# Kernel optimization log

Measured on AMD Instinct MI355X. Metric: run time of the kernel, lower is better.

The kernel has to match this reference:

```python
import jax, jax.numpy as jnp
import numpy as np

NEG = -9e15   # mask value used by reference pyGAT implementation
ALPHA = 0.2   # LeakyReLU negative slope
B, N, F_IN, H, F_HID = 131072, 8, 30, 3, 8


def setup_inputs() -> dict:
    key = jax.random.key(0)
    ks = jax.random.split(key, 14)
    x = jax.random.normal(ks[0], (B, N, F_IN), jnp.float32)
    adj = (jax.random.uniform(ks[1], (B, N, N)) > 0.5).astype(jnp.float32)
    adj = jnp.maximum(adj, jnp.eye(N, dtype=jnp.float32))  # self loops

    def init(k, shp, fan):
        return jax.random.normal(k, shp, jnp.float32) * np.float32(1.0 / np.sqrt(fan))

    return {
        "x": x,
        "adj": adj,
        "W_heads": init(ks[2], (H, F_IN, F_HID), F_IN),       # per-head W
        "a_heads": init(ks[3], (H, 2 * F_HID), 2 * F_HID),    # per-head attention vec
        "W_out": init(ks[4], (H * F_HID, 1), H * F_HID),      # out_att W (nclass=1)
        "a_out": init(ks[5], (2,), 2),                          # out_att attention vec
        "mu_W": init(ks[6], (8, 8), 8), "mu_b": jnp.zeros((8,), jnp.float32),
        "sg_W": init(ks[7], (8, 8), 8), "sg_b": jnp.zeros((8,), jnp.float32),
        "v_W": init(ks[8], (1, 8), 8), "v_b": jnp.zeros((1,), jnp.float32),
    }


def _gat(x, adj, W_heads, a_heads, W_out, a_out):
    # --- multi-head layer (concat=True) ---
    Wh = jnp.einsum('bnf,hfo->bhno', x, W_heads)            # [B,H,N,F_HID]
    a1, a2 = a_heads[:, :F_HID], a_heads[:, F_HID:]
    f1 = jnp.einsum('bhno,ho->bhn', Wh, a1)
    f2 = jnp.einsum('bhno,ho->bhn', Wh, a2)
    e = jax.nn.leaky_relu(f1[:, :, :, None] + f2[:, :, None, :], ALPHA)  # [B,H,N,N]
    e = jnp.where(adj[:, None, :, :] > 0, e, NEG)
    att = jax.nn.softmax(e, axis=-1)
    h = jax.nn.elu(jnp.einsum('bhnm,bhmo->bhno', att, Wh))  # [B,H,N,F_HID]
    h = h.transpose(0, 2, 1, 3).reshape(x.shape[0], N, H * F_HID)  # concat heads

    # --- output attention layer (concat=False, nclass=1) ---
    Wh2 = h @ W_out                                          # [B,N,1]
    g1 = Wh2[..., 0] * a_out[0]
    g2 = Wh2[..., 0] * a_out[1]
    e2 = jax.nn.leaky_relu(g1[:, :, None] + g2[:, None, :], ALPHA)  # [B,N,N]
    e2 = jnp.where(adj > 0, e2, NEG)
    att2 = jax.nn.softmax(e2, axis=-1)
    out = jnp.einsum('bnm,bmo->bno', att2, Wh2)              # [B,N,1]
    return jax.nn.elu(out)[..., 0]                            # squeeze(-1) -> [B,8]


def reference(x, adj, W_heads, a_heads, W_out, a_out,
              mu_W, mu_b, sg_W, sg_b, v_W, v_b):
    g = _gat(x, adj, W_heads, a_heads, W_out, a_out)          # [B,8]
    mu = jax.nn.sigmoid(g @ mu_W.T + mu_b)                    # [B,8]
    sigma = jax.nn.softplus(g @ sg_W.T + sg_b) + 0.001        # [B,8]
    value = g @ v_W.T + v_b                                   # [B,1]
    return (mu, sigma, value)
```

## Files before the change

### kernel.cpp

```cpp
#include <hip/hip_runtime.h>
#include <math.h>

#define TPB 512

constexpr int Bn    = 131072;
constexpr float LOG2E = 1.4426950408889634f;

typedef float v2f __attribute__((ext_vector_type(2)));

__global__ __launch_bounds__(TPB)
void gat_ppo_kernel(const float* __restrict__ xg,
                    const float* __restrict__ adjg,
                    const float* __restrict__ Wg,
                    const float* __restrict__ ahg,
                    const float* __restrict__ wog,
                    const float* __restrict__ aog,
                    const float* __restrict__ muWg,
                    const float* __restrict__ mubg,
                    const float* __restrict__ sgWg,
                    const float* __restrict__ sgbg,
                    const float* __restrict__ vWg,
                    const float* __restrict__ vbg,
                    float* __restrict__ outg)
{
    __shared__ float4 tile[8 * 200];

    const int lb = threadIdx.x;
    const int w  = lb >> 6;
    const int g  = (lb & 63) >> 3;
    const int n  = lb & 7;
    const size_t t = (size_t)blockIdx.x * TPB + lb;

    float4* wt4 = tile + w * 200;

    unsigned amask;
    {
        const float4* a4 = (const float4*)(adjg) + t * 2;
        float4 a0 = a4[0], a1 = a4[1];
        amask =  (unsigned)(a0.x > 0.0f)
              | ((unsigned)(a0.y > 0.0f) << 1)
              | ((unsigned)(a0.z > 0.0f) << 2)
              | ((unsigned)(a0.w > 0.0f) << 3)
              | ((unsigned)(a1.x > 0.0f) << 4)
              | ((unsigned)(a1.y > 0.0f) << 5)
              | ((unsigned)(a1.z > 0.0f) << 6)
              | ((unsigned)(a1.w > 0.0f) << 7);
    }

    float x[30];
    {
        const float2* xr = (const float2*)(xg + t * 30);
        #pragma unroll
        for (int k = 0; k < 15; ++k) {
            float2 v = xr[k];
            x[2 * k] = v.x; x[2 * k + 1] = v.y;
        }
    }

    const v2f* Wp = (const v2f*)Wg;
    float wh2 = 0.0f;

    #pragma unroll
    for (int h = 0; h < 3; ++h) {
        v2f acc[4];
        #pragma unroll
        for (int o2 = 0; o2 < 4; ++o2) acc[o2] = (v2f){0.0f, 0.0f};
        #pragma unroll
        for (int f = 0; f < 30; ++f) {
            v2f xf = (v2f){x[f], x[f]};
            #pragma unroll
            for (int o2 = 0; o2 < 4; ++o2)
                acc[o2] = __builtin_elementwise_fma(xf, Wp[h * 120 + f * 4 + o2], acc[o2]);
        }

        float s1 = 0.0f, s2 = 0.0f;
        #pragma unroll
        for (int o2 = 0; o2 < 4; ++o2) {
            s1 = fmaf(acc[o2].x, ahg[h * 16 + 2 * o2],     s1);
            s1 = fmaf(acc[o2].y, ahg[h * 16 + 2 * o2 + 1], s1);
            s2 = fmaf(acc[o2].x, ahg[h * 16 + 8 + 2 * o2],     s2);
            s2 = fmaf(acc[o2].y, ahg[h * 16 + 8 + 2 * o2 + 1], s2);
        }
        float f1h = s1 * LOG2E;
        float f2h = s2 * LOG2E;

        wt4[g * 25 + n * 3]     = (float4){acc[0].x, acc[0].y, acc[1].x, acc[1].y};
        wt4[g * 25 + n * 3 + 1] = (float4){acc[2].x, acc[2].y, acc[3].x, acc[3].y};

        float p[8];
        float s = 0.0f;
        #pragma unroll
        for (int m = 0; m < 8; ++m) {
            float ev = f1h + __shfl(f2h, m, 8);
            ev = fmaxf(ev, 0.2f * ev);
            float pe = ((amask >> m) & 1u) ? __builtin_amdgcn_exp2f(ev) : 0.0f;
            p[m] = pe; s += pe;
        }

        v2f hacc[4];
        #pragma unroll
        for (int o2 = 0; o2 < 4; ++o2) hacc[o2] = (v2f){0.0f, 0.0f};
        #pragma unroll
        for (int m = 0; m < 8; ++m) {
            float4 lo = wt4[g * 25 + m * 3];
            float4 hi = wt4[g * 25 + m * 3 + 1];
            v2f av = (v2f){p[m], p[m]};
            hacc[0] = __builtin_elementwise_fma(av, (v2f){lo.x, lo.y}, hacc[0]);
            hacc[1] = __builtin_elementwise_fma(av, (v2f){lo.z, lo.w}, hacc[1]);
            hacc[2] = __builtin_elementwise_fma(av, (v2f){hi.x, hi.y}, hacc[2]);
            hacc[3] = __builtin_elementwise_fma(av, (v2f){hi.z, hi.w}, hacc[3]);
        }
        float rs = 1.0f / s;
        #pragma unroll
        for (int o2 = 0; o2 < 4; ++o2) {
            #pragma unroll
            for (int j = 0; j < 2; ++j) {
                float hv = hacc[o2][j] * rs;
                hv = (hv > 0.0f) ? hv : (__expf(hv) - 1.0f);
                wh2 = fmaf(hv, wog[h * 8 + 2 * o2 + j], wh2);
            }
        }
    }

    const float a0c = aog[0] * LOG2E, a1c = aog[1] * LOG2E;
    float wh2a[8];
    #pragma unroll
    for (int m = 0; m < 8; ++m) wh2a[m] = __shfl(wh2, m, 8);

    float g1 = a0c * wh2;
    float s2s = 0.0f;
    float og = 0.0f;
    #pragma unroll
    for (int m = 0; m < 8; ++m) {
        float ev = fmaf(a1c, wh2a[m], g1);
        ev = fmaxf(ev, 0.2f * ev);
        float pe = ((amask >> m) & 1u) ? __builtin_amdgcn_exp2f(ev) : 0.0f;
        s2s += pe;
        og = fmaf(pe, wh2a[m], og);
    }
    og /= s2s;
    float g2v = (og > 0.0f) ? og : (__expf(og) - 1.0f);

    v2f gp[4];
    #pragma unroll
    for (int m = 0; m < 4; ++m)
        gp[m] = (v2f){__shfl(g2v, 2 * m, 8), __shfl(g2v, 2 * m + 1, 8)};

    const v2f* muWp = (const v2f*)muWg;
    const v2f* sgWp = (const v2f*)sgWg;
    const v2f* vWp  = (const v2f*)vWg;
    v2f ma = (v2f){0.0f, 0.0f}, sa = (v2f){0.0f, 0.0f}, va = (v2f){0.0f, 0.0f};
    #pragma unroll
    for (int k = 0; k < 4; ++k) {
        ma = __builtin_elementwise_fma(gp[k], muWp[n * 4 + k], ma);
        sa = __builtin_elementwise_fma(gp[k], sgWp[n * 4 + k], sa);
        va = __builtin_elementwise_fma(gp[k], vWp[k],          va);
    }
    float mu = ma.x + ma.y + mubg[n];
    float sg = sa.x + sa.y + sgbg[n];
    float vv = va.x + va.y + vbg[0];

    mu = 1.0f / (1.0f + __expf(-mu));
    sg = fmaxf(sg, 0.0f) + log1pf(__expf(-fabsf(sg))) + 0.001f;

    outg[t]          = mu;
    outg[Bn * 8 + t] = sg;
    if (n == 0) outg[Bn * 16 + (t >> 3)] = vv;
}

extern "C" void kernel_launch(void* const* d_in, const int* in_sizes, int n_in,
                              void* d_out, int out_size, void* d_ws, size_t ws_size,
                              hipStream_t stream) {
    const float* xg   = (const float*)d_in[0];
    const float* adjg = (const float*)d_in[1];
    const float* Wg   = (const float*)d_in[2];
    const float* ahg  = (const float*)d_in[3];
    const float* wog  = (const float*)d_in[4];
    const float* aog  = (const float*)d_in[5];
    const float* muW  = (const float*)d_in[6];
    const float* mub  = (const float*)d_in[7];
    const float* sgW  = (const float*)d_in[8];
    const float* sgb  = (const float*)d_in[9];
    const float* vW   = (const float*)d_in[10];
    const float* vb   = (const float*)d_in[11];
    float* outg = (float*)d_out;

    dim3 grid(Bn * 8 / TPB);
    gat_ppo_kernel<<<grid, TPB, 0, stream>>>(xg, adjg, Wg, ahg, wog, aog,
                                             muW, mub, sgW, sgb, vW, vb, outg);
}
```

Measured before the change: 51.85 us.

## Interleave all three heads per x element and halve block size

The per-head loop is restructured so each x element is loaded once and applied to all three heads' accumulators, with separate shared-memory tiles per head. The float x[30] register array disappears, and the softmax and aggregation phases run for all heads together, which exposes more independent work. Block size drops from 512 to 256 threads. The cost is more live accumulators (24 v2f in flight) and 3x the shared memory per wave, which may limit occupancy.

```diff
diff --git a/kernel.cpp b/kernel.cpp
--- a/kernel.cpp
+++ b/kernel.cpp
@@ -1,7 +1,7 @@
 #include <hip/hip_runtime.h>
 #include <math.h>
 
-#define TPB 512
+#define TPB 256
 
 constexpr int Bn    = 131072;
 constexpr float LOG2E = 1.4426950408889634f;
@@ -23,15 +23,13 @@
                     const float* __restrict__ vbg,
                     float* __restrict__ outg)
 {
-    __shared__ float4 tile[8 * 200];
+    __shared__ float4 tile[4][3][200];
 
     const int lb = threadIdx.x;
     const int w  = lb >> 6;
     const int g  = (lb & 63) >> 3;
     const int n  = lb & 7;
     const size_t t = (size_t)blockIdx.x * TPB + lb;
-
-    float4* wt4 = tile + w * 200;
 
     unsigned amask;
     {
@@ -47,75 +45,98 @@
               | ((unsigned)(a1.w > 0.0f) << 7);
     }
 
-    float x[30];
+    const v2f* Wp = (const v2f*)Wg;
+    v2f acc[3][4];
+    #pragma unroll
+    for (int h = 0; h < 3; ++h)
+        #pragma unroll
+        for (int o2 = 0; o2 < 4; ++o2) acc[h][o2] = (v2f){0.0f, 0.0f};
+
     {
         const float2* xr = (const float2*)(xg + t * 30);
         #pragma unroll
         for (int k = 0; k < 15; ++k) {
             float2 v = xr[k];
-            x[2 * k] = v.x; x[2 * k + 1] = v.y;
-        }
-    }
-
-    const v2f* Wp = (const v2f*)Wg;
+            #pragma unroll
+            for (int e = 0; e < 2; ++e) {
+                const int f = 2 * k + e;
+                const float xf = e ? v.y : v.x;
+                v2f xv = (v2f){xf, xf};
+                #pragma unroll
+                for (int h = 0; h < 3; ++h)
+                    #pragma unroll
+                    for (int o2 = 0; o2 < 4; ++o2)
+                        acc[h][o2] = __builtin_elementwise_fma(xv, Wp[h * 120 + f * 4 + o2], acc[h][o2]);
+            }
+        }
+    }
+
+    float f1h[3], f2h[3];
+    #pragma unroll
+    for (int h = 0; h < 3; ++h) {
+        float s1 = 0.0f, s2 = 0.0f;
+        #pragma unroll
+        for (int o2 = 0; o2 < 4; ++o2) {
+            s1 = fmaf(acc[h][o2].x, ahg[h * 16 + 2 * o2],     s1);
+            s1 = fmaf(acc[h][o2].y, ahg[h * 16 + 2 * o2 + 1], s1);
+            s2 = fmaf(acc[h][o2].x, ahg[h * 16 + 8 + 2 * o2],     s2);
+            s2 = fmaf(acc[h][o2].y, ahg[h * 16 + 8 + 2 * o2 + 1], s2);
+        }
+        f1h[h] = s1 * LOG2E;
+        f2h[h] = s2 * LOG2E;
+    }
+
+    #pragma unroll
+    for (int h = 0; h < 3; ++h) {
+        tile[w][h][g * 25 + n * 3]     = (float4){acc[h][0].x, acc[h][0].y, acc[h][1].x, acc[h][1].y};
+        tile[w][h][g * 25 + n * 3 + 1] = (float4){acc[h][2].x, acc[h][2].y, acc[h][3].x, acc[h][3].y};
+    }
+    asm volatile("" ::: "memory");
+    __builtin_amdgcn_sched_barrier(0);
+
+    float p[3][8];
+    float s[3] = {0.0f, 0.0f, 0.0f};
+    #pragma unroll
+    for (int m = 0; m < 8; ++m) {
+        const bool on = (amask >> m) & 1u;
+        #pragma unroll
+        for (int h = 0; h < 3; ++h) {
+            float ev = f1h[h] + __shfl(f2h[h], m, 8);
+            ev = fmaxf(ev, 0.2f * ev);
+            float pe = on ? __builtin_amdgcn_exp2f(ev) : 0.0f;
+            p[h][m] = pe; s[h] += pe;
+        }
+    }
+
+    v2f hacc[3][4];
+    #pragma unroll
+    for (int h = 0; h < 3; ++h)
+        #pragma unroll
+        for (int o2 = 0; o2 < 4; ++o2) hacc[h][o2] = (v2f){0.0f, 0.0f};
+
+    #pragma unroll
+    for (int m = 0; m < 8; ++m) {
+        #pragma unroll
+        for (int h = 0; h < 3; ++h) {
+            float4 lo = tile[w][h][g * 25 + m * 3];
+            float4 hi = tile[w][h][g * 25 + m * 3 + 1];
+            v2f av = (v2f){p[h][m], p[h][m]};
+            hacc[h][0] = __builtin_elementwise_fma(av, (v2f){lo.x, lo.y}, hacc[h][0]);
+            hacc[h][1] = __builtin_elementwise_fma(av, (v2f){lo.z, lo.w}, hacc[h][1]);
+            hacc[h][2] = __builtin_elementwise_fma(av, (v2f){hi.x, hi.y}, hacc[h][2]);
+            hacc[h][3] = __builtin_elementwise_fma(av, (v2f){hi.z, hi.w}, hacc[h][3]);
+        }
+    }
+
     float wh2 = 0.0f;
-
     #pragma unroll
     for (int h = 0; h < 3; ++h) {
-        v2f acc[4];
-        #pragma unroll
-        for (int o2 = 0; o2 < 4; ++o2) acc[o2] = (v2f){0.0f, 0.0f};
-        #pragma unroll
-        for (int f = 0; f < 30; ++f) {
-            v2f xf = (v2f){x[f], x[f]};
-            #pragma unroll
-            for (int o2 = 0; o2 < 4; ++o2)
-                acc[o2] = __builtin_elementwise_fma(xf, Wp[h * 120 + f * 4 + o2], acc[o2]);
-        }
-
-        float s1 = 0.0f, s2 = 0.0f;
-        #pragma unroll
-        for (int o2 = 0; o2 < 4; ++o2) {
-            s1 = fmaf(acc[o2].x, ahg[h * 16 + 2 * o2],     s1);
-            s1 = fmaf(acc[o2].y, ahg[h * 16 + 2 * o2 + 1], s1);
-            s2 = fmaf(acc[o2].x, ahg[h * 16 + 8 + 2 * o2],     s2);
-            s2 = fmaf(acc[o2].y, ahg[h * 16 + 8 + 2 * o2 + 1], s2);
-        }
-        float f1h = s1 * LOG2E;
-        float f2h = s2 * LOG2E;
-
-        wt4[g * 25 + n * 3]     = (float4){acc[0].x, acc[0].y, acc[1].x, acc[1].y};
-        wt4[g * 25 + n * 3 + 1] = (float4){acc[2].x, acc[2].y, acc[3].x, acc[3].y};
-
-        float p[8];
-        float s = 0.0f;
-        #pragma unroll
-        for (int m = 0; m < 8; ++m) {
-            float ev = f1h + __shfl(f2h, m, 8);
-            ev = fmaxf(ev, 0.2f * ev);
-            float pe = ((amask >> m) & 1u) ? __builtin_amdgcn_exp2f(ev) : 0.0f;
-            p[m] = pe; s += pe;
-        }
-
-        v2f hacc[4];
-        #pragma unroll
-        for (int o2 = 0; o2 < 4; ++o2) hacc[o2] = (v2f){0.0f, 0.0f};
-        #pragma unroll
-        for (int m = 0; m < 8; ++m) {
-            float4 lo = wt4[g * 25 + m * 3];
-            float4 hi = wt4[g * 25 + m * 3 + 1];
-            v2f av = (v2f){p[m], p[m]};
-            hacc[0] = __builtin_elementwise_fma(av, (v2f){lo.x, lo.y}, hacc[0]);
-            hacc[1] = __builtin_elementwise_fma(av, (v2f){lo.z, lo.w}, hacc[1]);
-            hacc[2] = __builtin_elementwise_fma(av, (v2f){hi.x, hi.y}, hacc[2]);
-            hacc[3] = __builtin_elementwise_fma(av, (v2f){hi.z, hi.w}, hacc[3]);
-        }
-        float rs = 1.0f / s;
+        float rs = 1.0f / s[h];
         #pragma unroll
         for (int o2 = 0; o2 < 4; ++o2) {
             #pragma unroll
             for (int j = 0; j < 2; ++j) {
-                float hv = hacc[o2][j] * rs;
+                float hv = hacc[h][o2][j] * rs;
                 hv = (hv > 0.0f) ? hv : (__expf(hv) - 1.0f);
                 wh2 = fmaf(hv, wog[h * 8 + 2 * o2 + j], wh2);
             }
```

Measured after the change: 49.08 us, median of 2. 5.3% less time.
